# Performance work log

Measured on AMD Instinct MI355X. Metric: run time of the kernel, lower is better.

The kernel has to match this reference:

```python
import jax, jax.numpy as jnp
import numpy as np

N_NODES = 100000
N_EDGES = 1600000
DIM = 128


def setup_inputs() -> dict:
    key = jax.random.key(0)
    k1, k2, k3, k4 = jax.random.split(key, 4)
    x = jax.random.normal(k1, (N_NODES, DIM), dtype=jnp.float32)
    edge_index = jax.random.randint(k2, (2, N_EDGES), 0, N_NODES, dtype=jnp.int64)
    scale = 1.0 / np.sqrt(DIM)
    W1 = jax.random.normal(k3, (DIM, DIM), dtype=jnp.float32) * scale
    W2 = jax.random.normal(k4, (DIM, DIM), dtype=jnp.float32) * scale
    b1 = jnp.zeros((DIM,), dtype=jnp.float32)
    b2 = jnp.zeros((DIM,), dtype=jnp.float32)
    return {"x": x, "edge_index": edge_index, "W1": W1, "b1": b1, "W2": W2, "b2": b2}


def _gcn_conv(x, src, dst, dinv, W, b, n):
    # linear transform first (PyG GCNConv), then normalized scatter-add aggregation
    h = x @ W                                   # [N, out]
    norm = dinv[src] * dinv[dst]                # [E+N]
    msg = h[src] * norm[:, None]                # [E+N, out]
    agg = jax.ops.segment_sum(msg, dst, num_segments=n)
    return agg + b


def reference(x, edge_index, W1, b1, W2, b2):
    n = x.shape[0]
    loops = jnp.arange(n, dtype=edge_index.dtype)
    src = jnp.concatenate([edge_index[0], loops])  # add self-loops
    dst = jnp.concatenate([edge_index[1], loops])
    deg = jax.ops.segment_sum(jnp.ones_like(src, dtype=x.dtype), dst, num_segments=n)
    dinv = jnp.where(deg > 0, jax.lax.rsqrt(deg), 0.0)  # D^{-1/2}
    h = _gcn_conv(x, src, dst, dinv, W1, b1, n)
    h = jax.nn.relu(h)
    out = _gcn_conv(h, src, dst, dinv, W2, b2, n)
    return out
```

## Files before the change

kernel.cpp:

```cpp
#include <hip/hip_runtime.h>
#include <hip/hip_bf16.h>
#include <hip/hip_fp16.h>

#define NN 100000
#define DIM 128
#define NB 391
#define BCAP 5120
#define GTILES ((NN + 63) / 64)
#define STP 130

typedef _Float16 f16x8 __attribute__((ext_vector_type(8)));
typedef float f32x4 __attribute__((ext_vector_type(4)));

__global__ void k_init(const float* __restrict__ W1, const float* __restrict__ W2,
                       int* __restrict__ bcur, _Float16* __restrict__ Wt1,
                       _Float16* __restrict__ Wt2) {
    const int b = blockIdx.x;
    const int t = threadIdx.x;
    if (b < 2) {
        const int i = b * 256 + t;
        if (i < NB) bcur[i] = 0;
        return;
    }
    const int idx = (b - 2) * 256 + t;
    const int which = idx >> 14;
    const int i = idx & 16383;
    const int n = i >> 7, k = i & 127;
    if (which == 0) Wt1[n * DIM + k] = (_Float16)W1[k * DIM + n];
    else            Wt2[n * DIM + k] = (_Float16)W2[k * DIM + n];
}

__global__ void k_binA(const int* __restrict__ src, const int* __restrict__ dst,
                       int* __restrict__ bcur, int* __restrict__ binbuf, int E) {
    __shared__ int hist[4][NB];
    const int t  = threadIdx.x;
    const int wv = t >> 6;
    for (int i = t; i < 4 * NB; i += 256) ((int*)hist)[i] = 0;
    __syncthreads();

    const int e0 = blockIdx.x * 4096;
    int mys[16], myd[16];
#pragma unroll
    for (int i = 0; i < 16; ++i) {
        const int e = e0 + i * 256 + t;
        int d = -1, s = 0;
        if (e < E) {
            d = dst[e];
            s = src[e];
            atomicAdd(&hist[wv][d >> 8], 1);
        }
        mys[i] = s;
        myd[i] = d;
    }
    __syncthreads();

    for (int b = t; b < NB; b += 256) {
        const int h0 = hist[0][b], h1 = hist[1][b], h2 = hist[2][b], h3 = hist[3][b];
        const int tot = h0 + h1 + h2 + h3;
        const int base = tot ? atomicAdd(&bcur[b], tot) : 0;
        hist[0][b] = base;
        hist[1][b] = base + h0;
        hist[2][b] = base + h0 + h1;
        hist[3][b] = base + h0 + h1 + h2;
    }
    __syncthreads();

#pragma unroll
    for (int i = 0; i < 16; ++i) {
        const int d = myd[i];
        if (d >= 0) {
            const int b = d >> 8;
            const int p = atomicAdd(&hist[wv][b], 1);
            if (p < BCAP) binbuf[b * BCAP + p] = mys[i] | ((d & 255) << 17);
        }
    }
}

__global__ void k_scan2(const int* __restrict__ bcur, int* __restrict__ bbase, int nb) {
    __shared__ int s[512];
    const int t = threadIdx.x;
    const int v = (t < nb) ? bcur[t] : 0;
    s[t] = v;
    __syncthreads();
    int acc = v;
    for (int d = 1; d < 512; d <<= 1) {
        const int o = (t >= d) ? s[t - d] : 0;
        __syncthreads();
        acc += o;
        s[t] = acc;
        __syncthreads();
    }
    if (t < nb) bbase[t] = acc - v;
}

__global__ void k_gemm1(const float* __restrict__ inF, const _Float16* __restrict__ Wt,
                        _Float16* __restrict__ outH, const int* __restrict__ bbase,
                        const int* __restrict__ bcur, const int* __restrict__ binbuf,
                        int* __restrict__ rowptr, float* __restrict__ dinv,
                        int* __restrict__ csr) {
    __shared__ int cnt4[4][256];
    __shared__ int sc[256];
    __shared__ _Float16 st[64][STP];
    const int t  = threadIdx.x;
    const int wv = t >> 6;

    if (blockIdx.x < NB) {
        const int b = blockIdx.x;
        const int node = b * 256 + t;
#pragma unroll
        for (int w = 0; w < 4; ++w) cnt4[w][t] = 0;
        __syncthreads();
        const int n_e = min(bcur[b], BCAP);
        const int* p = &binbuf[b * BCAP];
        for (int i = t; i < n_e; i += 256) atomicAdd(&cnt4[wv][p[i] >> 17], 1);
        __syncthreads();
        const int c0 = cnt4[0][t], c1 = cnt4[1][t], c2 = cnt4[2][t], c3 = cnt4[3][t];
        const int c = c0 + c1 + c2 + c3;
        if (node < NN) dinv[node] = rsqrtf((float)(c + 1));
        sc[t] = c;
        __syncthreads();
        int acc = c;
        for (int d = 1; d < 256; d <<= 1) {
            const int o = (t >= d) ? sc[t - d] : 0;
            __syncthreads();
            acc += o;
            sc[t] = acc;
            __syncthreads();
        }
        const int ex = acc - c + bbase[b];
        if (node < NN) {
            rowptr[node] = ex;
            if (node == NN - 1) rowptr[NN] = ex + c;
        }
        cnt4[0][t] = ex;
        cnt4[1][t] = ex + c0;
        cnt4[2][t] = ex + c0 + c1;
        cnt4[3][t] = ex + c0 + c1 + c2;
        __syncthreads();
        for (int i = t; i < n_e; i += 256) {
            const int v = p[i];
            const int pos = atomicAdd(&cnt4[wv][v >> 17], 1);
            csr[pos] = v & 0x1FFFF;
        }
        return;
    }

    const int tile = blockIdx.x - NB;
    const int row0 = tile * 64;
    const int l    = t & 63;
    const int l15  = l & 15;
    const int lk8  = (l >> 4) << 3;
    const int colw = wv << 5;

    f16x8 bf[2][4];
#pragma unroll
    for (int ct = 0; ct < 2; ++ct)
#pragma unroll
        for (int kt = 0; kt < 4; ++kt)
            bf[ct][kt] = *(const f16x8*)&Wt[(colw + ct * 16 + l15) * DIM + kt * 32 + lk8];

    f32x4 acc[4][2];
#pragma unroll
    for (int rt = 0; rt < 4; ++rt)
#pragma unroll
        for (int ct = 0; ct < 2; ++ct) acc[rt][ct] = (f32x4){0.f, 0.f, 0.f, 0.f};

#pragma unroll
    for (int rt = 0; rt < 4; ++rt) {
        int row = row0 + rt * 16 + l15;
        row = min(row, NN - 1);
        f16x8 a[4];
#pragma unroll
        for (int kt = 0; kt < 4; ++kt) {
            const int k0 = kt * 32 + lk8;
            const float4 v0 = *(const float4*)&inF[row * DIM + k0];
            const float4 v1 = *(const float4*)&inF[row * DIM + k0 + 4];
            f16x8 v;
            v[0] = (_Float16)v0.x; v[1] = (_Float16)v0.y;
            v[2] = (_Float16)v0.z; v[3] = (_Float16)v0.w;
            v[4] = (_Float16)v1.x; v[5] = (_Float16)v1.y;
            v[6] = (_Float16)v1.z; v[7] = (_Float16)v1.w;
            a[kt] = v;
        }
#pragma unroll
        for (int ct = 0; ct < 2; ++ct)
#pragma unroll
            for (int kt = 0; kt < 4; ++kt)
                acc[rt][ct] = __builtin_amdgcn_mfma_f32_16x16x32_f16(a[kt], bf[ct][kt],
                                                                    acc[rt][ct], 0, 0, 0);
    }

#pragma unroll
    for (int rt = 0; rt < 4; ++rt)
#pragma unroll
        for (int r = 0; r < 4; ++r) {
            const int lr = rt * 16 + ((l >> 4) << 2) + r;
            st[lr][colw + l15]      = (_Float16)acc[rt][0][r];
            st[lr][colw + 16 + l15] = (_Float16)acc[rt][1][r];
        }
    __syncthreads();
#pragma unroll
    for (int i = 0; i < 4; ++i) {
        const int lr  = (wv << 4) + (i << 2) + (l >> 4);
        const int row = row0 + lr;
        if (row < NN) {
            const uint4 v = *(const uint4*)&st[lr][l15 << 3];
            *(uint4*)&outH[row * DIM + (l15 << 3)] = v;
        }
    }
}

__global__ void k_gemm2(const _Float16* __restrict__ inH, const _Float16* __restrict__ Wt,
                        const float* __restrict__ dinv, _Float16* __restrict__ outH) {
    __shared__ _Float16 st[64][STP];
    const int t = threadIdx.x;
    const int row0 = blockIdx.x * 64;
    const int wv   = t >> 6;
    const int l    = t & 63;
    const int l15  = l & 15;
    const int lk8  = (l >> 4) << 3;
    const int colw = wv << 5;

    f16x8 bf[2][4];
#pragma unroll
    for (int ct = 0; ct < 2; ++ct)
#pragma unroll
        for (int kt = 0; kt < 4; ++kt)
            bf[ct][kt] = *(const f16x8*)&Wt[(colw + ct * 16 + l15) * DIM + kt * 32 + lk8];

    f32x4 acc[4][2];
#pragma unroll
    for (int rt = 0; rt < 4; ++rt)
#pragma unroll
        for (int ct = 0; ct < 2; ++ct) acc[rt][ct] = (f32x4){0.f, 0.f, 0.f, 0.f};

#pragma unroll
    for (int rt = 0; rt < 4; ++rt) {
        int row = row0 + rt * 16 + l15;
        row = min(row, NN - 1);
        f16x8 a[4];
#pragma unroll
        for (int kt = 0; kt < 4; ++kt)
            a[kt] = *(const f16x8*)&inH[row * DIM + kt * 32 + lk8];
#pragma unroll
        for (int ct = 0; ct < 2; ++ct)
#pragma unroll
            for (int kt = 0; kt < 4; ++kt)
                acc[rt][ct] = __builtin_amdgcn_mfma_f32_16x16x32_f16(a[kt], bf[ct][kt],
                                                                    acc[rt][ct], 0, 0, 0);
    }

#pragma unroll
    for (int rt = 0; rt < 4; ++rt)
#pragma unroll
        for (int r = 0; r < 4; ++r) {
            const int lr = rt * 16 + ((l >> 4) << 2) + r;
            const float d = dinv[min(row0 + lr, NN - 1)];
            st[lr][colw + l15]      = (_Float16)(acc[rt][0][r] * d);
            st[lr][colw + 16 + l15] = (_Float16)(acc[rt][1][r] * d);
        }
    __syncthreads();
#pragma unroll
    for (int i = 0; i < 4; ++i) {
        const int lr  = (wv << 4) + (i << 2) + (l >> 4);
        const int row = row0 + lr;
        if (row < NN) {
            const uint4 v = *(const uint4*)&st[lr][l15 << 3];
            *(uint4*)&outH[row * DIM + (l15 << 3)] = v;
        }
    }
}

__global__ void k_gather1(const _Float16* __restrict__ hsp, _Float16* __restrict__ aggH,
                          const int* __restrict__ csr, const int* __restrict__ rowptr,
                          const float* __restrict__ dinv, const float* __restrict__ bias) {
    const __half* __restrict__ hs = (const __half*)hsp;
    const int w = (blockIdx.x * blockDim.x + threadIdx.x) >> 6;
    if (w >= NN) return;
    const int lane = threadIdx.x & 63;
    const int off  = lane << 1;

    const int start = __builtin_amdgcn_readfirstlane(rowptr[w]);
    const int end   = __builtin_amdgcn_readfirstlane(rowptr[w + 1]);
    const float dw  = dinv[w];

    float2 a0 = {0.f, 0.f}, a1 = {0.f, 0.f}, a2 = {0.f, 0.f}, a3 = {0.f, 0.f};
    {
        const float2 v = __half22float2(*(const __half2*)&hs[w * DIM + off]);
        a0.x = dw * v.x; a0.y = dw * v.y;
    }

    int j = start;
    for (; j + 7 < end; j += 8) {
        const int s0 = __builtin_amdgcn_readfirstlane(csr[j]);
        const int s1 = __builtin_amdgcn_readfirstlane(csr[j + 1]);
        const int s2 = __builtin_amdgcn_readfirstlane(csr[j + 2]);
        const int s3 = __builtin_amdgcn_readfirstlane(csr[j + 3]);
        const int s4 = __builtin_amdgcn_readfirstlane(csr[j + 4]);
        const int s5 = __builtin_amdgcn_readfirstlane(csr[j + 5]);
        const int s6 = __builtin_amdgcn_readfirstlane(csr[j + 6]);
        const int s7 = __builtin_amdgcn_readfirstlane(csr[j + 7]);
        const float d0 = dinv[s0], d1 = dinv[s1], d2 = dinv[s2], d3 = dinv[s3];
        const float d4 = dinv[s4], d5 = dinv[s5], d6 = dinv[s6], d7 = dinv[s7];
        const float2 v0 = __half22float2(*(const __half2*)&hs[s0 * DIM + off]);
        const float2 v1 = __half22float2(*(const __half2*)&hs[s1 * DIM + off]);
        const float2 v2 = __half22float2(*(const __half2*)&hs[s2 * DIM + off]);
        const float2 v3 = __half22float2(*(const __half2*)&hs[s3 * DIM + off]);
        const float2 v4 = __half22float2(*(const __half2*)&hs[s4 * DIM + off]);
        const float2 v5 = __half22float2(*(const __half2*)&hs[s5 * DIM + off]);
        const float2 v6 = __half22float2(*(const __half2*)&hs[s6 * DIM + off]);
        const float2 v7 = __half22float2(*(const __half2*)&hs[s7 * DIM + off]);
        a0.x = fmaf(d0, v0.x, a0.x); a0.y = fmaf(d0, v0.y, a0.y);
        a1.x = fmaf(d1, v1.x, a1.x); a1.y = fmaf(d1, v1.y, a1.y);
        a2.x = fmaf(d2, v2.x, a2.x); a2.y = fmaf(d2, v2.y, a2.y);
        a3.x = fmaf(d3, v3.x, a3.x); a3.y = fmaf(d3, v3.y, a3.y);
        a0.x = fmaf(d4, v4.x, a0.x); a0.y = fmaf(d4, v4.y, a0.y);
        a1.x = fmaf(d5, v5.x, a1.x); a1.y = fmaf(d5, v5.y, a1.y);
        a2.x = fmaf(d6, v6.x, a2.x); a2.y = fmaf(d6, v6.y, a2.y);
        a3.x = fmaf(d7, v7.x, a3.x); a3.y = fmaf(d7, v7.y, a3.y);
    }
    for (; j < end; ++j) {
        const int s0 = __builtin_amdgcn_readfirstlane(csr[j]);
        const float d0 = dinv[s0];
        const float2 v0 = __half22float2(*(const __half2*)&hs[s0 * DIM + off]);
        a0.x = fmaf(d0, v0.x, a0.x); a0.y = fmaf(d0, v0.y, a0.y);
    }

    const float2 bb = {bias[off], bias[off + 1]};
    float2 r = {a0.x + a1.x + a2.x + a3.x, a0.y + a1.y + a2.y + a3.y};
    r.x = fmaxf(fmaf(dw, r.x, bb.x), 0.f);
    r.y = fmaxf(fmaf(dw, r.y, bb.y), 0.f);
    *(__half2*)&aggH[w * DIM + off] = __floats2half2_rn(r.x, r.y);
}

__global__ void k_gather2(const _Float16* __restrict__ hsp, float* __restrict__ outF,
                          const int* __restrict__ csr, const int* __restrict__ rowptr,
                          const float* __restrict__ dinv, const float* __restrict__ bias) {
    const __half* __restrict__ hs = (const __half*)hsp;
    const int w = (blockIdx.x * blockDim.x + threadIdx.x) >> 6;
    if (w >= NN) return;
    const int lane = threadIdx.x & 63;
    const int off  = lane << 1;

    const int start = __builtin_amdgcn_readfirstlane(rowptr[w]);
    const int end   = __builtin_amdgcn_readfirstlane(rowptr[w + 1]);

    float2 a0 = __half22float2(*(const __half2*)&hs[w * DIM + off]);
    float2 a1 = {0.f, 0.f}, a2 = {0.f, 0.f}, a3 = {0.f, 0.f};

    int j = start;
    for (; j + 7 < end; j += 8) {
        const int s0 = __builtin_amdgcn_readfirstlane(csr[j]);
        const int s1 = __builtin_amdgcn_readfirstlane(csr[j + 1]);
        const int s2 = __builtin_amdgcn_readfirstlane(csr[j + 2]);
        const int s3 = __builtin_amdgcn_readfirstlane(csr[j + 3]);
        const int s4 = __builtin_amdgcn_readfirstlane(csr[j + 4]);
        const int s5 = __builtin_amdgcn_readfirstlane(csr[j + 5]);
        const int s6 = __builtin_amdgcn_readfirstlane(csr[j + 6]);
        const int s7 = __builtin_amdgcn_readfirstlane(csr[j + 7]);
        const float2 v0 = __half22float2(*(const __half2*)&hs[s0 * DIM + off]);
        const float2 v1 = __half22float2(*(const __half2*)&hs[s1 * DIM + off]);
        const float2 v2 = __half22float2(*(const __half2*)&hs[s2 * DIM + off]);
        const float2 v3 = __half22float2(*(const __half2*)&hs[s3 * DIM + off]);
        const float2 v4 = __half22float2(*(const __half2*)&hs[s4 * DIM + off]);
        const float2 v5 = __half22float2(*(const __half2*)&hs[s5 * DIM + off]);
        const float2 v6 = __half22float2(*(const __half2*)&hs[s6 * DIM + off]);
        const float2 v7 = __half22float2(*(const __half2*)&hs[s7 * DIM + off]);
        a0.x += v0.x; a0.y += v0.y;
        a1.x += v1.x; a1.y += v1.y;
        a2.x += v2.x; a2.y += v2.y;
        a3.x += v3.x; a3.y += v3.y;
        a0.x += v4.x; a0.y += v4.y;
        a1.x += v5.x; a1.y += v5.y;
        a2.x += v6.x; a2.y += v6.y;
        a3.x += v7.x; a3.y += v7.y;
    }
    for (; j < end; ++j) {
        const int s0 = __builtin_amdgcn_readfirstlane(csr[j]);
        const float2 v0 = __half22float2(*(const __half2*)&hs[s0 * DIM + off]);
        a0.x += v0.x; a0.y += v0.y;
    }

    const float d = dinv[w];
    const float2 bb = {bias[off], bias[off + 1]};
    float2 r = {a0.x + a1.x + a2.x + a3.x, a0.y + a1.y + a2.y + a3.y};
    float2 o;
    o.x = fmaf(d, r.x, bb.x);
    o.y = fmaf(d, r.y, bb.y);
    *(float2*)&outF[w * DIM + off] = o;
}

extern "C" void kernel_launch(void* const* d_in, const int* in_sizes, int n_in,
                              void* d_out, int out_size, void* d_ws, size_t ws_size,
                              hipStream_t stream) {
    const float* x  = (const float*)d_in[0];
    const int*   ei = (const int*)d_in[1];
    const float* W1 = (const float*)d_in[2];
    const float* b1 = (const float*)d_in[3];
    const float* W2 = (const float*)d_in[4];
    const float* b2 = (const float*)d_in[5];
    float* out = (float*)d_out;

    const int E = in_sizes[1] / 2;
    const int* src = ei;
    const int* dst = ei + E;

    char* ws = (char*)d_ws;
    float*    dinv   = (float*)(ws);
    int*      rowptr = (int*)  (ws + (2  << 20));
    int*      bbase  = (int*)  (ws + (3  << 20));
    int*      bcur   = (int*)  (ws + (3  << 20) + 65536);
    _Float16* Wt1    = (_Float16*)(ws + (3 << 20) + 131072);
    _Float16* Wt2    = (_Float16*)(ws + (3 << 20) + 196608);
    int*      csr    = (int*)  (ws + (4  << 20));
    int*      binbuf = (int*)  (ws + (11 << 20));
    _Float16* hs     = (_Float16*)(ws + (20 << 20));
    _Float16* aggH   = (_Float16*)(ws + (47 << 20));
    _Float16* hs2    = (_Float16*)(ws + (74 << 20));

    const int ABLK = (E + 4095) / 4096;

    k_init <<<130, 256, 0, stream>>>(W1, W2, bcur, Wt1, Wt2);
    k_binA <<<ABLK, 256, 0, stream>>>(src, dst, bcur, binbuf, E);
    k_scan2<<<1, 512, 0, stream>>>(bcur, bbase, NB);

    k_gemm1<<<NB + GTILES, 256, 0, stream>>>(x, Wt1, hs, bbase, bcur, binbuf,
                                             rowptr, dinv, csr);
    k_gather1<<<(NN * 64) / 256, 256, 0, stream>>>(hs, aggH, csr, rowptr, dinv, b1);

    k_gemm2<<<GTILES, 256, 0, stream>>>(aggH, Wt2, dinv, hs2);
    k_gather2<<<(NN * 64) / 256, 256, 0, stream>>>(hs2, out, csr, rowptr, dinv, b2);
}
```

Baseline: 225.7 us.

## Fuse edge binning with first GEMM and replace scan kernel with atomic CSR allocation

Edge binning now runs in the same launch as the first GEMM, so the binning blocks overlap with the MFMA tiles. The separate single-block scan kernel is dropped. Each bin's CSR segment is instead claimed through an atomic global cursor inside a new fill kernel, and rows are described by separate rowstart and rowend arrays. This removes one launch and a serial scan step, but the CSR segments are no longer in node order, and the fill work now runs as its own kernel after the GEMM.

```diff
diff --git a/kernel.cpp b/kernel.cpp
--- a/kernel.cpp
+++ b/kernel.cpp
@@ -19,7 +19,7 @@
     const int t = threadIdx.x;
     if (b < 2) {
         const int i = b * 256 + t;
-        if (i < NB) bcur[i] = 0;
+        if (i <= NB) bcur[i] = 0;
         return;
     }
     const int idx = (b - 2) * 256 + t;
@@ -30,122 +30,59 @@
     else            Wt2[n * DIM + k] = (_Float16)W2[k * DIM + n];
 }
 
-__global__ void k_binA(const int* __restrict__ src, const int* __restrict__ dst,
-                       int* __restrict__ bcur, int* __restrict__ binbuf, int E) {
+__global__ void k_binA_gemm1(const float* __restrict__ inF, const _Float16* __restrict__ Wt,
+                             _Float16* __restrict__ outH, const int* __restrict__ src,
+                             const int* __restrict__ dst, int* __restrict__ bcur,
+                             int* __restrict__ binbuf, int E, int nbin) {
     __shared__ int hist[4][NB];
-    const int t  = threadIdx.x;
-    const int wv = t >> 6;
-    for (int i = t; i < 4 * NB; i += 256) ((int*)hist)[i] = 0;
-    __syncthreads();
-
-    const int e0 = blockIdx.x * 4096;
-    int mys[16], myd[16];
-#pragma unroll
-    for (int i = 0; i < 16; ++i) {
-        const int e = e0 + i * 256 + t;
-        int d = -1, s = 0;
-        if (e < E) {
-            d = dst[e];
-            s = src[e];
-            atomicAdd(&hist[wv][d >> 8], 1);
-        }
-        mys[i] = s;
-        myd[i] = d;
-    }
-    __syncthreads();
-
-    for (int b = t; b < NB; b += 256) {
-        const int h0 = hist[0][b], h1 = hist[1][b], h2 = hist[2][b], h3 = hist[3][b];
-        const int tot = h0 + h1 + h2 + h3;
-        const int base = tot ? atomicAdd(&bcur[b], tot) : 0;
-        hist[0][b] = base;
-        hist[1][b] = base + h0;
-        hist[2][b] = base + h0 + h1;
-        hist[3][b] = base + h0 + h1 + h2;
-    }
-    __syncthreads();
-
-#pragma unroll
-    for (int i = 0; i < 16; ++i) {
-        const int d = myd[i];
-        if (d >= 0) {
-            const int b = d >> 8;
-            const int p = atomicAdd(&hist[wv][b], 1);
-            if (p < BCAP) binbuf[b * BCAP + p] = mys[i] | ((d & 255) << 17);
-        }
-    }
-}
-
-__global__ void k_scan2(const int* __restrict__ bcur, int* __restrict__ bbase, int nb) {
-    __shared__ int s[512];
-    const int t = threadIdx.x;
-    const int v = (t < nb) ? bcur[t] : 0;
-    s[t] = v;
-    __syncthreads();
-    int acc = v;
-    for (int d = 1; d < 512; d <<= 1) {
-        const int o = (t >= d) ? s[t - d] : 0;
-        __syncthreads();
-        acc += o;
-        s[t] = acc;
-        __syncthreads();
-    }
-    if (t < nb) bbase[t] = acc - v;
-}
-
-__global__ void k_gemm1(const float* __restrict__ inF, const _Float16* __restrict__ Wt,
-                        _Float16* __restrict__ outH, const int* __restrict__ bbase,
-                        const int* __restrict__ bcur, const int* __restrict__ binbuf,
-                        int* __restrict__ rowptr, float* __restrict__ dinv,
-                        int* __restrict__ csr) {
-    __shared__ int cnt4[4][256];
-    __shared__ int sc[256];
     __shared__ _Float16 st[64][STP];
     const int t  = threadIdx.x;
     const int wv = t >> 6;
 
-    if (blockIdx.x < NB) {
-        const int b = blockIdx.x;
-        const int node = b * 256 + t;
-#pragma unroll
-        for (int w = 0; w < 4; ++w) cnt4[w][t] = 0;
+    if ((int)blockIdx.x < nbin) {
+        for (int i = t; i < 4 * NB; i += 256) ((int*)hist)[i] = 0;
         __syncthreads();
-        const int n_e = min(bcur[b], BCAP);
-        const int* p = &binbuf[b * BCAP];
-        for (int i = t; i < n_e; i += 256) atomicAdd(&cnt4[wv][p[i] >> 17], 1);
+
+        const int e0 = blockIdx.x * 4096;
+        int mys[16], myd[16];
+#pragma unroll
+        for (int i = 0; i < 16; ++i) {
+            const int e = e0 + i * 256 + t;
+            int d = -1, s = 0;
+            if (e < E) {
+                d = dst[e];
+                s = src[e];
+                atomicAdd(&hist[wv][d >> 8], 1);
+            }
+            mys[i] = s;
+            myd[i] = d;
+        }
         __syncthreads();
-        const int c0 = cnt4[0][t], c1 = cnt4[1][t], c2 = cnt4[2][t], c3 = cnt4[3][t];
-        const int c = c0 + c1 + c2 + c3;
-        if (node < NN) dinv[node] = rsqrtf((float)(c + 1));
-        sc[t] = c;
+
+        for (int b = t; b < NB; b += 256) {
+            const int h0 = hist[0][b], h1 = hist[1][b], h2 = hist[2][b], h3 = hist[3][b];
+            const int tot = h0 + h1 + h2 + h3;
+            const int base = tot ? atomicAdd(&bcur[b], tot) : 0;
+            hist[0][b] = base;
+            hist[1][b] = base + h0;
+            hist[2][b] = base + h0 + h1;
+            hist[3][b] = base + h0 + h1 + h2;
+        }
         __syncthreads();
-        int acc = c;
-        for (int d = 1; d < 256; d <<= 1) {
-            const int o = (t >= d) ? sc[t - d] : 0;
-            __syncthreads();
-            acc += o;
-            sc[t] = acc;
-            __syncthreads();
-        }
-        const int ex = acc - c + bbase[b];
-        if (node < NN) {
-            rowptr[node] = ex;
-            if (node == NN - 1) rowptr[NN] = ex + c;
-        }
-        cnt4[0][t] = ex;
-        cnt4[1][t] = ex + c0;
-        cnt4[2][t] = ex + c0 + c1;
-        cnt4[3][t] = ex + c0 + c1 + c2;
-        __syncthreads();
-        for (int i = t; i < n_e; i += 256) {
-            const int v = p[i];
-            const int pos = atomicAdd(&cnt4[wv][v >> 17], 1);
-            csr[pos] = v & 0x1FFFF;
+
+#pragma unroll
+        for (int i = 0; i < 16; ++i) {
+            const int d = myd[i];
+            if (d >= 0) {
+                const int b = d >> 8;
+                const int p = atomicAdd(&hist[wv][b], 1);
+                if (p < BCAP) binbuf[b * BCAP + p] = mys[i] | ((d & 255) << 17);
+            }
         }
         return;
     }
 
-    const int tile = blockIdx.x - NB;
+    const int tile = blockIdx.x - nbin;
     const int row0 = tile * 64;
     const int l    = t & 63;
     const int l15  = l & 15;
@@ -210,78 +147,70 @@
     }
 }
 
-__global__ void k_gemm2(const _Float16* __restrict__ inH, const _Float16* __restrict__ Wt,
-                        const float* __restrict__ dinv, _Float16* __restrict__ outH) {
-    __shared__ _Float16 st[64][STP];
-    const int t = threadIdx.x;
-    const int row0 = blockIdx.x * 64;
-    const int wv   = t >> 6;
-    const int l    = t & 63;
-    const int l15  = l & 15;
-    const int lk8  = (l >> 4) << 3;
-    const int colw = wv << 5;
-
-    f16x8 bf[2][4];
-#pragma unroll
-    for (int ct = 0; ct < 2; ++ct)
-#pragma unroll
-        for (int kt = 0; kt < 4; ++kt)
-            bf[ct][kt] = *(const f16x8*)&Wt[(colw + ct * 16 + l15) * DIM + kt * 32 + lk8];
-
-    f32x4 acc[4][2];
-#pragma unroll
-    for (int rt = 0; rt < 4; ++rt)
-#pragma unroll
-        for (int ct = 0; ct < 2; ++ct) acc[rt][ct] = (f32x4){0.f, 0.f, 0.f, 0.f};
-
-#pragma unroll
-    for (int rt = 0; rt < 4; ++rt) {
-        int row = row0 + rt * 16 + l15;
-        row = min(row, NN - 1);
-        f16x8 a[4];
-#pragma unroll
-        for (int kt = 0; kt < 4; ++kt)
-            a[kt] = *(const f16x8*)&inH[row * DIM + kt * 32 + lk8];
-#pragma unroll
-        for (int ct = 0; ct < 2; ++ct)
-#pragma unroll
-            for (int kt = 0; kt < 4; ++kt)
-                acc[rt][ct] = __builtin_amdgcn_mfma_f32_16x16x32_f16(a[kt], bf[ct][kt],
-                                                                    acc[rt][ct], 0, 0, 0);
-    }
-
-#pragma unroll
-    for (int rt = 0; rt < 4; ++rt)
-#pragma unroll
-        for (int r = 0; r < 4; ++r) {
-            const int lr = rt * 16 + ((l >> 4) << 2) + r;
-            const float d = dinv[min(row0 + lr, NN - 1)];
-            st[lr][colw + l15]      = (_Float16)(acc[rt][0][r] * d);
-            st[lr][colw + 16 + l15] = (_Float16)(acc[rt][1][r] * d);
-        }
-    __syncthreads();
-#pragma unroll
-    for (int i = 0; i < 4; ++i) {
-        const int lr  = (wv << 4) + (i << 2) + (l >> 4);
-        const int row = row0 + lr;
-        if (row < NN) {
-            const uint4 v = *(const uint4*)&st[lr][l15 << 3];
-            *(uint4*)&outH[row * DIM + (l15 << 3)] = v;
-        }
+__global__ void k_fill(const int* __restrict__ bcur, const int* __restrict__ binbuf,
+                       int* __restrict__ gcur, float* __restrict__ dinv,
+                       int* __restrict__ rowstart, int* __restrict__ rowend,
+                       int* __restrict__ csr) {
+    __shared__ int cnt4[4][256];
+    __shared__ int sc[256];
+    __shared__ int sbase;
+    const int b  = blockIdx.x;
+    const int t  = threadIdx.x;
+    const int wv = t >> 6;
+
+#pragma unroll
+    for (int w = 0; w < 4; ++w) cnt4[w][t] = 0;
+    __syncthreads();
+    const int n_e = min(bcur[b], BCAP);
+    const int* p = &binbuf[b * BCAP];
+    for (int i = t; i < n_e; i += 256) atomicAdd(&cnt4[wv][p[i] >> 17], 1);
+    __syncthreads();
+    const int c0 = cnt4[0][t], c1 = cnt4[1][t], c2 = cnt4[2][t], c3 = cnt4[3][t];
+    const int c = c0 + c1 + c2 + c3;
+    sc[t] = c;
+    __syncthreads();
+    int acc = c;
+    for (int d = 1; d < 256; d <<= 1) {
+        const int o = (t >= d) ? sc[t - d] : 0;
+        __syncthreads();
+        acc += o;
+        sc[t] = acc;
+        __syncthreads();
+    }
+    if (t == 0) sbase = atomicAdd(gcur, sc[255]);
+    __syncthreads();
+    const int ex = acc - c + sbase;
+
+    const int node = b * 256 + t;
+    if (node < NN) {
+        rowstart[node] = ex;
+        rowend[node]   = ex + c;
+        dinv[node]     = rsqrtf((float)(c + 1));
+    }
+    cnt4[0][t] = ex;
+    cnt4[1][t] = ex + c0;
+    cnt4[2][t] = ex + c0 + c1;
+    cnt4[3][t] = ex + c0 + c1 + c2;
+    __syncthreads();
+    for (int i = t; i < n_e; i += 256) {
+        const int v = p[i];
+        const int pos = atomicAdd(&cnt4[wv][v >> 17], 1);
+        csr[pos] = v & 0x1FFFF;
     }
 }
 
 __global__ void k_gather1(const _Float16* __restrict__ hsp, _Float16* __restrict__ aggH,
-                          const int* __restrict__ csr, const int* __restrict__ rowptr,
-                          const float* __restrict__ dinv, const float* __restrict__ bias) {
+                          const int* __restrict__ csr, const int* __restrict__ rowstart,
+                          const int* __restrict__ rowend, const float* __restrict__ dinv,
+                          const float* __restrict__ bias) {
     const __half* __restrict__ hs = (const __half*)hsp;
     const int w = (blockIdx.x * blockDim.x + threadIdx.x) >> 6;
     if (w >= NN) return;
     const int lane = threadIdx.x & 63;
     const int off  = lane << 1;
 
-    const int start = __builtin_amdgcn_readfirstlane(rowptr[w]);
-    const int end   = __builtin_amdgcn_readfirstlane(rowptr[w + 1]);
+    const int start = __builtin_amdgcn_readfirstlane(rowstart[w]);
+    const int end   = __builtin_amdgcn_readfirstlane(rowend[w]);
     const float dw  = dinv[w];
 
     float2 a0 = {0.f, 0.f}, a1 = {0.f, 0.f}, a2 = {0.f, 0.f}, a3 = {0.f, 0.f};
@@ -333,17 +262,79 @@
     *(__half2*)&aggH[w * DIM + off] = __floats2half2_rn(r.x, r.y);
 }
 
+__global__ void k_gemm2(const _Float16* __restrict__ inH, const _Float16* __restrict__ Wt,
+                        const float* __restrict__ dinv, _Float16* __restrict__ outH) {
+    __shared__ _Float16 st[64][STP];
+    const int t = threadIdx.x;
+    const int row0 = blockIdx.x * 64;
+    const int wv   = t >> 6;
+    const int l    = t & 63;
+    const int l15  = l & 15;
+    const int lk8  = (l >> 4) << 3;
+    const int colw = wv << 5;
+
+    f16x8 bf[2][4];
+#pragma unroll
+    for (int ct = 0; ct < 2; ++ct)
+#pragma unroll
+        for (int kt = 0; kt < 4; ++kt)
+            bf[ct][kt] = *(const f16x8*)&Wt[(colw + ct * 16 + l15) * DIM + kt * 32 + lk8];
+
+    f32x4 acc[4][2];
+#pragma unroll
+    for (int rt = 0; rt < 4; ++rt)
+#pragma unroll
+        for (int ct = 0; ct < 2; ++ct) acc[rt][ct] = (f32x4){0.f, 0.f, 0.f, 0.f};
+
+#pragma unroll
+    for (int rt = 0; rt < 4; ++rt) {
+        int row = row0 + rt * 16 + l15;
+        row = min(row, NN - 1);
+        f16x8 a[4];
+#pragma unroll
+        for (int kt = 0; kt < 4; ++kt)
+            a[kt] = *(const f16x8*)&inH[row * DIM + kt * 32 + lk8];
+#pragma unroll
+        for (int ct = 0; ct < 2; ++ct)
+#pragma unroll
+            for (int kt = 0; kt < 4; ++kt)
+                acc[rt][ct] = __builtin_amdgcn_mfma_f32_16x16x32_f16(a[kt], bf[ct][kt],
+                                                                    acc[rt][ct], 0, 0, 0);
+    }
+
+#pragma unroll
+    for (int rt = 0; rt < 4; ++rt)
+#pragma unroll
+        for (int r = 0; r < 4; ++r) {
+            const int lr = rt * 16 + ((l >> 4) << 2) + r;
+            const float d = dinv[min(row0 + lr, NN - 1)];
+            st[lr][colw + l15]      = (_Float16)(acc[rt][0][r] * d);
+            st[lr][colw + 16 + l15] = (_Float16)(acc[rt][1][r] * d);
+        }
+    __syncthreads();
+#pragma unroll
+    for (int i = 0; i < 4; ++i) {
+        const int lr  = (wv << 4) + (i << 2) + (l >> 4);
+        const int row = row0 + lr;
+        if (row < NN) {
+            const uint4 v = *(const uint4*)&st[lr][l15 << 3];
+            *(uint4*)&outH[row * DIM + (l15 << 3)] = v;
+        }
+    }
+}
+
 __global__ void k_gather2(const _Float16* __restrict__ hsp, float* __restrict__ outF,
-                          const int* __restrict__ csr, const int* __restrict__ rowptr,
-                          const float* __restrict__ dinv, const float* __restrict__ bias) {
+                          const int* __restrict__ csr, const int* __restrict__ rowstart,
+                          const int* __restrict__ rowend, const float* __restrict__ dinv,
+                          const float* __restrict__ bias) {
     const __half* __restrict__ hs = (const __half*)hsp;
     const int w = (blockIdx.x * blockDim.x + threadIdx.x) >> 6;
     if (w >= NN) return;
     const int lane = threadIdx.x & 63;
     const int off  = lane << 1;
 
-    const int start = __builtin_amdgcn_readfirstlane(rowptr[w]);
-    const int end   = __builtin_amdgcn_readfirstlane(rowptr[w + 1]);
+    const int start = __builtin_amdgcn_readfirstlane(rowstart[w]);
+    const int end   = __builtin_amdgcn_readfirstlane(rowend[w]);
 
     float2 a0 = __half22float2(*(const __half2*)&hs[w * DIM + off]);
     float2 a1 = {0.f, 0.f}, a2 = {0.f, 0.f}, a3 = {0.f, 0.f};
@@ -406,28 +397,32 @@
     const int* dst = ei + E;
 
     char* ws = (char*)d_ws;
-    float*    dinv   = (float*)(ws);
-    int*      rowptr = (int*)  (ws + (2  << 20));
-    int*      bbase  = (int*)  (ws + (3  << 20));
-    int*      bcur   = (int*)  (ws + (3  << 20) + 65536);
-    _Float16* Wt1    = (_Float16*)(ws + (3 << 20) + 131072);
-    _Float16* Wt2    = (_Float16*)(ws + (3 << 20) + 196608);
-    int*      csr    = (int*)  (ws + (4  << 20));
-    int*      binbuf = (int*)  (ws + (11 << 20));
-    _Float16* hs     = (_Float16*)(ws + (20 << 20));
-    _Float16* aggH   = (_Float16*)(ws + (47 << 20));
-    _Float16* hs2    = (_Float16*)(ws + (74 << 20));
+    float*    dinv     = (float*)(ws);
+    int*      rowstart = (int*)  (ws + (1 << 20));
+    int*      rowend   = (int*)  (ws + (1 << 20) + 524288);
+    int*      bcur     = (int*)  (ws + (2 << 20));
+    _Float16* Wt1      = (_Float16*)(ws + (2 << 20) + 65536);
+    _Float16* Wt2      = (_Float16*)(ws + (2 << 20) + 131072);
+    int*      csr      = (int*)  (ws + (4  << 20));
+    int*      binbuf   = (int*)  (ws + (11 << 20));
+    _Float16* hs       = (_Float16*)(ws + (20 << 20));
+    _Float16* aggH     = (_Float16*)(ws + (47 << 20));
+    _Float16* hs2      = (_Float16*)(ws + (74 << 20));
+    int*      gcur     = bcur + NB;
 
     const int ABLK = (E + 4095) / 4096;
 
-    k_init <<<130, 256, 0, stream>>>(W1, W2, bcur, Wt1, Wt2);
-    k_binA <<<ABLK, 256, 0, stream>>>(src, dst, bcur, binbuf, E);
-    k_scan2<<<1, 512, 0, stream>>>(bcur, bbase, NB);
-
-    k_gemm1<<<NB + GTILES, 256, 0, stream>>>(x, Wt1, hs, bbase, bcur, binbuf,
-                                             rowptr, dinv, csr);
-    k_gather1<<<(NN * 64) / 256, 256, 0, stream>>>(hs, aggH, csr, rowptr, dinv, b1);
+    k_init<<<130, 256, 0, stream>>>(W1, W2, bcur, Wt1, Wt2);
+
+    k_binA_gemm1<<<ABLK + GTILES, 256, 0, stream>>>(x, Wt1, hs, src, dst, bcur,
+                                                    binbuf, E, ABLK);
+
+    k_fill<<<NB, 256, 0, stream>>>(bcur, binbuf, gcur, dinv, rowstart, rowend, csr);
+
+    k_gather1<<<(NN * 64) / 256, 256, 0, stream>>>(hs, aggH, csr, rowstart, rowend,
+                                                   dinv, b1);
 
     k_gemm2<<<GTILES, 256, 0, stream>>>(aggH, Wt2, dinv, hs2);
-    k_gather2<<<(NN * 64) / 256, 256, 0, stream>>>(hs2, out, csr, rowptr, dinv, b2);
-}
+    k_gather2<<<(NN * 64) / 256, 256, 0, stream>>>(hs2, out, csr, rowstart, rowend,
+                                                   dinv, b2);
+}
```

New measurement: 225.8 us. Within noise of the previous version (+0.1%).
